# Performance work log

Hardware: AMD Instinct MI355X
Metric: run time of the kernel (lower is better)

Reference implementation:

```python
import jax, jax.numpy as jnp
import numpy as np

D_MODEL = 1024
NUM_HEADS = 16
D_HEAD = D_MODEL // NUM_HEADS
B, S = 4, 2048


def setup_inputs() -> dict:
    key = jax.random.key(0)
    ks = jax.random.split(key, 11)
    s = 1.0 / np.sqrt(D_MODEL)
    inp = {
        "query": jax.random.normal(ks[0], (B, S, D_MODEL), jnp.float32),
        "key": jax.random.normal(ks[1], (B, S, D_MODEL), jnp.float32),
        "value": jax.random.normal(ks[2], (B, S, D_MODEL), jnp.float32),
        "Wq": jax.random.uniform(ks[3], (D_MODEL, D_MODEL), jnp.float32, -s, s),
        "bq": jax.random.uniform(ks[4], (D_MODEL,), jnp.float32, -s, s),
        "Wk": jax.random.uniform(ks[5], (D_MODEL, D_MODEL), jnp.float32, -s, s),
        "bk": jax.random.uniform(ks[6], (D_MODEL,), jnp.float32, -s, s),
        "Wv": jax.random.uniform(ks[7], (D_MODEL, D_MODEL), jnp.float32, -s, s),
        "bv": jax.random.uniform(ks[8], (D_MODEL,), jnp.float32, -s, s),
        "Wo": jax.random.uniform(ks[9], (D_MODEL, D_MODEL), jnp.float32, -s, s),
        "bo": jax.random.uniform(ks[10], (D_MODEL,), jnp.float32, -s, s),
    }
    return inp


def reference(query, key, value, Wq, bq, Wk, bk, Wv, bv, Wo, bo):
    # Linear projections (torch Linear: x @ W.T + b)
    q = query @ Wq.T + bq  # [B,S,D]
    k = key @ Wk.T + bk
    v = value @ Wv.T + bv
    # split heads -> [B,H,S,Dh]
    def split(x):
        return x.reshape(B, S, NUM_HEADS, D_HEAD).transpose(0, 2, 1, 3)
    q, k, v = split(q), split(k), split(v)
    scale = 1.0 / np.sqrt(D_HEAD).astype(np.float32)
    scores = jnp.einsum('bhqd,bhkd->bhqk', q, k) * scale
    attn = jax.nn.softmax(scores, axis=-1)  # dropout is identity in eval
    ctx = jnp.einsum('bhqk,bhkd->bhqd', attn, v)
    ctx = ctx.transpose(0, 2, 1, 3).reshape(B, S, D_MODEL)
    return ctx @ Wo.T + bo
```

## Files before the change

kernel.cpp:

```cpp
#include <hip/hip_runtime.h>
#include <hip/hip_bf16.h>

typedef __bf16 bf16;
typedef bf16 bf16x8 __attribute__((ext_vector_type(8)));
typedef float f32x4 __attribute__((ext_vector_type(4)));
typedef float f32x16 __attribute__((ext_vector_type(16)));
typedef unsigned int u32x2 __attribute__((ext_vector_type(2)));
typedef unsigned int u32x4 __attribute__((ext_vector_type(4)));

#define B_  4
#define S_  2048
#define DM  1024
#define NH  16
#define DH  64

#define QSCALE 0.18033688011112042f


__device__ __forceinline__ void async_copy16(const void* g, void* lds) {
    __builtin_amdgcn_global_load_lds(
        (const __attribute__((address_space(1))) void*)g,
        (__attribute__((address_space(3))) void*)lds,
        16, 0, 0);
}

__device__ __forceinline__ bf16x8 read_frag(const char* lds, int row, int kbyte) {
    int off = row * 128 + (kbyte ^ ((row & 7) << 4));
    return *(const bf16x8*)(lds + off);
}

template<int ROWS, int NT>
__device__ __forceinline__ void stage_g2l(const bf16* g, int gs, char* lds) {
    int t = threadIdx.x;
#pragma unroll
    for (int i = 0; i < ROWS * 8 / NT; ++i) {
        int c = i * NT + t;
        int r = c >> 3;
        int s = (c & 7) ^ (r & 7);
        async_copy16(g + (long)r * gs + s * 8, lds + c * 16);
    }
}

__device__ __forceinline__ void stage_f32_g2l(const float* g, int gs, char* lds) {
    int t = threadIdx.x;
#pragma unroll
    for (int i = 0; i < 8; ++i) {
        int c = i * 256 + t;
        int r = c >> 4;
        int ch = c & 15;
        int sch = ch ^ (r & 15);
        async_copy16(g + (long)r * gs + sch * 4, lds + c * 16);
    }
}

__device__ __forceinline__ unsigned cvt_pk(float lo, float hi) {
    unsigned r;
    asm("v_cvt_pk_bf16_f32 %0, %1, %2" : "=v"(r) : "v"(lo), "v"(hi));
    return r;
}

__device__ __forceinline__ bf16x8 read_frag_f32(const char* lds, int row, int ks, int seg) {
    int ch0 = ks * 8 + seg * 2;
    int sw = row & 15;
    const char* base = lds + row * 256;
    f32x4 lo = *(const f32x4*)(base + ((ch0 ^ sw) * 16));
    f32x4 hi = *(const f32x4*)(base + (((ch0 + 1) ^ sw) * 16));
    u32x4 w;
    w.x = cvt_pk(lo[0], lo[1]);
    w.y = cvt_pk(lo[2], lo[3]);
    w.z = cvt_pk(hi[0], hi[1]);
    w.w = cvt_pk(hi[2], hi[3]);
    return __builtin_bit_cast(bf16x8, w);
}

__device__ __forceinline__ u32x2 pl32swap(unsigned a, unsigned b) {
    return __builtin_amdgcn_permlane32_swap(a, b, false, false);
}


__device__ __forceinline__ void cvt_body(const float* __restrict__ s, bf16* __restrict__ d, int n8) {
    for (int i = blockIdx.x * 256 + threadIdx.x; i < n8; i += gridDim.x * 256) {
        f32x4 v0 = *(const f32x4*)(s + (long)i * 8);
        f32x4 v1 = *(const f32x4*)(s + (long)i * 8 + 4);
        bf16x8 r;
#pragma unroll
        for (int j = 0; j < 4; ++j) { r[j] = (bf16)v0[j]; r[j + 4] = (bf16)v1[j]; }
        *(bf16x8*)(d + (long)i * 8) = r;
    }
}

__global__ __launch_bounds__(256) void cvt_w(
    const float* __restrict__ a, const float* __restrict__ b,
    const float* __restrict__ c, const float* __restrict__ d,
    bf16* __restrict__ oa, bf16* __restrict__ ob, bf16* __restrict__ oc, bf16* __restrict__ od)
{
    int z = blockIdx.y;
    cvt_body(z == 0 ? a : z == 1 ? b : z == 2 ? c : d,
             z == 0 ? oa : z == 1 ? ob : z == 2 ? oc : od, DM * DM / 8);
}

__global__ __launch_bounds__(256) void qkv_gemm(
    const float* __restrict__ xq, const float* __restrict__ xk, const float* __restrict__ xv,
    const bf16* __restrict__ wq, const bf16* __restrict__ wk, const bf16* __restrict__ wv,
    const float* __restrict__ bq, const float* __restrict__ bk, const float* __restrict__ bv,
    bf16* __restrict__ qo, bf16* __restrict__ ko, bf16* __restrict__ vo)
{
    __shared__ alignas(128) char As[128 * 256];
    __shared__ alignas(128) char Bs[128 * 128];

    int z = blockIdx.y;
    const float* X    = (z == 0) ? xq : (z == 1) ? xk : xv;
    const bf16* W     = (z == 0) ? wq : (z == 1) ? wk : wv;
    const float* bias = (z == 0) ? bq : (z == 1) ? bk : bv;
    bf16* out         = (z == 0) ? qo : (z == 1) ? ko : vo;
    float scale       = (z == 0) ? QSCALE : 1.0f;
    bool  vt          = (z == 2);

    int p = blockIdx.x;
    int xcd = p & 7, slot = p >> 3;
    int m0 = (xcd * 8 + (slot >> 3)) * 128;
    int n0 = (slot & 7) * 128;

    int lane = threadIdx.x & 63, wid = threadIdx.x >> 6;
    int wm = (wid >> 1) * 64, wn = (wid & 1) * 64;
    int seg = lane >> 4;

    f32x4 acc[4][4];
#pragma unroll
    for (int i = 0; i < 4; ++i)
#pragma unroll
        for (int j = 0; j < 4; ++j) acc[i][j] = f32x4{0.f, 0.f, 0.f, 0.f};

    for (int k0 = 0; k0 < DM; k0 += 64) {
        __syncthreads();
        stage_f32_g2l(X + (long)m0 * DM + k0, DM, As);
        stage_g2l<128, 256>(W + (long)n0 * DM + k0, DM, Bs);
        __syncthreads();
#pragma unroll
        for (int ks = 0; ks < 2; ++ks) {
            int kb = ks * 64 + seg * 16;
            bf16x8 af[4], bfr[4];
#pragma unroll
            for (int f = 0; f < 4; ++f)
                af[f] = read_frag_f32(As, wm + f * 16 + (lane & 15), ks, seg);
#pragma unroll
            for (int f = 0; f < 4; ++f)
                bfr[f] = read_frag(Bs, wn + f * 16 + (lane & 15), kb);
#pragma unroll
            for (int mf = 0; mf < 4; ++mf)
#pragma unroll
                for (int nf = 0; nf < 4; ++nf)
                    acc[mf][nf] = __builtin_amdgcn_mfma_f32_16x16x32_bf16(
                        af[mf], bfr[nf], acc[mf][nf], 0, 0, 0);
        }
    }

#pragma unroll
    for (int nf = 0; nf < 4; ++nf) {
        int j = n0 + wn + nf * 16 + (lane & 15);
        float bj = bias[j];
        int h = j >> 6, dh = j & 63;
#pragma unroll
        for (int mf = 0; mf < 4; ++mf) {
#pragma unroll
            for (int r = 0; r < 4; ++r) {
                int i = m0 + wm + mf * 16 + (lane >> 4) * 4 + r;
                float v = (acc[mf][nf][r] + bj) * scale;
                int b = i >> 11, s = i & 2047;
                long addr = vt ? ((long)((b * NH + h) * DH + dh)) * S_ + s
                               : ((long)((b * NH + h) * S_ + s)) * DH + dh;
                out[addr] = (bf16)v;
            }
        }
    }
}

__global__ __launch_bounds__(256) void out_gemm(
    const bf16* __restrict__ ctxb, const bf16* __restrict__ wo, const float* __restrict__ bo,
    float* __restrict__ out)
{
    __shared__ alignas(128) char As[128 * 128];
    __shared__ alignas(128) char Bs[128 * 128];

    int p = blockIdx.x;
    int xcd = p & 7, slot = p >> 3;
    int m0 = (xcd * 8 + (slot >> 3)) * 128;
    int n0 = (slot & 7) * 128;

    int lane = threadIdx.x & 63, wid = threadIdx.x >> 6;
    int wm = (wid >> 1) * 64, wn = (wid & 1) * 64;

    f32x4 acc[4][4];
#pragma unroll
    for (int i = 0; i < 4; ++i)
#pragma unroll
        for (int j = 0; j < 4; ++j) acc[i][j] = f32x4{0.f, 0.f, 0.f, 0.f};

    for (int k0 = 0; k0 < DM; k0 += 64) {
        __syncthreads();
        stage_g2l<128, 256>(ctxb + (long)m0 * DM + k0, DM, As);
        stage_g2l<128, 256>(wo + (long)n0 * DM + k0, DM, Bs);
        __syncthreads();
#pragma unroll
        for (int ks = 0; ks < 2; ++ks) {
            int kb = ks * 64 + (lane >> 4) * 16;
            bf16x8 af[4], bfr[4];
#pragma unroll
            for (int f = 0; f < 4; ++f) af[f]  = read_frag(As, wm + f * 16 + (lane & 15), kb);
#pragma unroll
            for (int f = 0; f < 4; ++f) bfr[f] = read_frag(Bs, wn + f * 16 + (lane & 15), kb);
#pragma unroll
            for (int mf = 0; mf < 4; ++mf)
#pragma unroll
                for (int nf = 0; nf < 4; ++nf)
                    acc[mf][nf] = __builtin_amdgcn_mfma_f32_16x16x32_bf16(
                        af[mf], bfr[nf], acc[mf][nf], 0, 0, 0);
        }
    }

#pragma unroll
    for (int nf = 0; nf < 4; ++nf) {
        int j = n0 + wn + nf * 16 + (lane & 15);
        float bj = bo[j];
#pragma unroll
        for (int mf = 0; mf < 4; ++mf)
#pragma unroll
            for (int r = 0; r < 4; ++r) {
                int i = m0 + wm + mf * 16 + (lane >> 4) * 4 + r;
                out[(long)i * DM + j] = acc[mf][nf][r] + bj;
            }
    }
}

__global__ __launch_bounds__(256) void attn_fwd(
    const bf16* __restrict__ qb, const bf16* __restrict__ kb, const bf16* __restrict__ vtb,
    bf16* __restrict__ ctx)
{
    __shared__ alignas(128) char Ks[2][64 * 128];
    __shared__ alignas(128) char Vs[2][64 * 128];

    int bid = blockIdx.x;
    int xcd = bid & 7, rest = bid >> 3;
    int qt = rest & 15, bh = xcd + 8 * (rest >> 4);

    int lane = threadIdx.x & 63, wid = threadIdx.x >> 6;
    int ln = lane & 31, h = lane >> 5;
    int q0w = qt * 128 + wid * 32;

    const bf16* qg = qb + (long)bh * S_ * DH;
    const bf16* kg = kb + (long)bh * S_ * DH;
    const bf16* vg = vtb + (long)bh * DH * S_;

    bf16x8 qf[4];
#pragma unroll
    for (int s = 0; s < 4; ++s)
        qf[s] = *(const bf16x8*)(qg + (long)(q0w + ln) * DH + s * 16 + h * 8);

    const bf16x8 onea = __builtin_bit_cast(bf16x8,
        u32x4{0x3F803F80u, 0x3F803F80u, 0x3F803F80u, 0x3F803F80u});

    f32x16 fz;
#pragma unroll
    for (int r = 0; r < 16; ++r) fz[r] = 0.f;

    f32x16 o[2];
#pragma unroll
    for (int t = 0; t < 2; ++t)
#pragma unroll
        for (int r = 0; r < 16; ++r) o[t][r] = 0.f;
    f32x16 lacc;
#pragma unroll
    for (int r = 0; r < 16; ++r) lacc[r] = 0.f;

    stage_g2l<64, 256>(kg, DH, Ks[0]);
    stage_g2l<64, 256>(vg, S_, Vs[0]);
    __syncthreads();

    int cur = 0;
    for (int kt2 = 0; kt2 < S_ / 64; ++kt2) {
        f32x16 acc[2];
        __builtin_amdgcn_s_setprio(1);
#pragma unroll
        for (int t = 0; t < 2; ++t) {
            bf16x8 ka = read_frag(Ks[cur], 32 * t + ln, 16 * h);
            acc[t] = __builtin_amdgcn_mfma_f32_32x32x16_bf16(ka, qf[0], fz, 0, 0, 0);
        }
#pragma unroll
        for (int s = 1; s < 4; ++s)
#pragma unroll
            for (int t = 0; t < 2; ++t) {
                bf16x8 ka = read_frag(Ks[cur], 32 * t + ln, 32 * s + 16 * h);
                acc[t] = __builtin_amdgcn_mfma_f32_32x32x16_bf16(ka, qf[s], acc[t], 0, 0, 0);
            }
        __builtin_amdgcn_s_setprio(0);

        if (kt2 + 1 < S_ / 64) {
            stage_g2l<64, 256>(kg + (long)(kt2 + 1) * 64 * DH, DH, Ks[cur ^ 1]);
            stage_g2l<64, 256>(vg + (kt2 + 1) * 64, S_, Vs[cur ^ 1]);
        }

#pragma unroll
        for (int t = 0; t < 2; ++t)
#pragma unroll
            for (int r = 0; r < 16; ++r)
                acc[t][r] = __builtin_amdgcn_exp2f(acc[t][r]);

        unsigned pf[4][4];
#pragma unroll
        for (int t = 0; t < 2; ++t)
#pragma unroll
            for (int hf = 0; hf < 2; ++hf) {
                int rb = 8 * hf;
                unsigned a0 = cvt_pk(acc[t][rb + 0], acc[t][rb + 1]);
                unsigned s0 = cvt_pk(acc[t][rb + 4], acc[t][rb + 5]);
                unsigned a1 = cvt_pk(acc[t][rb + 2], acc[t][rb + 3]);
                unsigned s1 = cvt_pk(acc[t][rb + 6], acc[t][rb + 7]);
                u32x2 r0 = pl32swap(a0, s0);
                u32x2 r1 = pl32swap(a1, s1);
                int kt = 2 * t + hf;
                pf[kt][0] = r0.x; pf[kt][2] = r0.y;
                pf[kt][1] = r1.x; pf[kt][3] = r1.y;
            }

        __builtin_amdgcn_s_setprio(1);
#pragma unroll
        for (int kt = 0; kt < 4; ++kt) {
            bf16x8 pb = __builtin_bit_cast(bf16x8,
                u32x4{pf[kt][0], pf[kt][1], pf[kt][2], pf[kt][3]});
            bf16x8 va0 = read_frag(Vs[cur], ln,      32 * kt + 16 * h);
            o[0] = __builtin_amdgcn_mfma_f32_32x32x16_bf16(va0, pb, o[0], 0, 0, 0);
            bf16x8 va1 = read_frag(Vs[cur], 32 + ln, 32 * kt + 16 * h);
            o[1] = __builtin_amdgcn_mfma_f32_32x32x16_bf16(va1, pb, o[1], 0, 0, 0);
            lacc = __builtin_amdgcn_mfma_f32_32x32x16_bf16(onea, pb, lacc, 0, 0, 0);
        }
        __builtin_amdgcn_s_setprio(0);

        __syncthreads();
        cur ^= 1;
    }

    int b = bh >> 4, head = bh & 15;
    float inv = 1.0f / lacc[0];
    int s = q0w + ln;
    bf16* base = ctx + ((long)(b * S_ + s)) * DM + head * DH;
#pragma unroll
    for (int dt = 0; dt < 2; ++dt)
#pragma unroll
        for (int c = 0; c < 4; ++c) {
            int d0 = 32 * dt + 8 * c + 4 * h;
            u32x2 st;
            st.x = cvt_pk(o[dt][4 * c + 0] * inv, o[dt][4 * c + 1] * inv);
            st.y = cvt_pk(o[dt][4 * c + 2] * inv, o[dt][4 * c + 3] * inv);
            *(u32x2*)(base + d0) = st;
        }
}

extern "C" void kernel_launch(void* const* d_in, const int* in_sizes, int n_in,
                              void* d_out, int out_size, void* d_ws, size_t ws_size,
                              hipStream_t stream) {
    const float* query = (const float*)d_in[0];
    const float* key   = (const float*)d_in[1];
    const float* value = (const float*)d_in[2];
    const float* Wq = (const float*)d_in[3];
    const float* bq = (const float*)d_in[4];
    const float* Wk = (const float*)d_in[5];
    const float* bk = (const float*)d_in[6];
    const float* Wv = (const float*)d_in[7];
    const float* bv = (const float*)d_in[8];
    const float* Wo = (const float*)d_in[9];
    const float* bo = (const float*)d_in[10];
    float* out = (float*)d_out;

    char* ws = (char*)d_ws;
    const long MB = 1ll << 20;
    bf16* qb   = (bf16*)(ws + 0 * MB);
    bf16* kb   = (bf16*)(ws + 16 * MB);
    bf16* vtb  = (bf16*)(ws + 32 * MB);
    bf16* ctxb = (bf16*)(ws + 48 * MB);
    bf16* wqb  = (bf16*)(ws + 64 * MB);
    bf16* wkb  = (bf16*)(ws + 66 * MB);
    bf16* wvb  = (bf16*)(ws + 68 * MB);
    bf16* wob  = (bf16*)(ws + 70 * MB);

    dim3 blk(256);
    cvt_w<<<dim3(512, 4), blk, 0, stream>>>(Wq, Wk, Wv, Wo, wqb, wkb, wvb, wob);
    qkv_gemm<<<dim3(512, 3), blk, 0, stream>>>(query, key, value, wqb, wkb, wvb,
                                               bq, bk, bv, qb, kb, vtb);
    attn_fwd<<<dim3(1024), blk, 0, stream>>>(qb, kb, vtb, ctxb);
    out_gemm<<<dim3(512), blk, 0, stream>>>(ctxb, wob, bo, out);
}
```

Baseline: 215.8 us.

## Software-pipeline attention loop: compute next QK^T while doing current PV

Restructures the attention main loop so the QK^T MFMAs for tile t+1 are issued alongside the PV MFMAs for tile t. The exp2 and bf16 packing of the next tile then happen after the barrier, and the prefetch is issued two tiles ahead into the freed buffer. The aim is to overlap the exp/convert VALU work and the load latency with matrix-core work. In exchange it needs more registers for the extra accumulator set, which could lower occupancy.

New measurement: 209.4 us, median of 2. -2.9%, faster.

```diff
diff --git a/kernel.cpp b/kernel.cpp
--- a/kernel.cpp
+++ b/kernel.cpp
@@ -275,54 +275,67 @@
     stage_g2l<64, 256>(kg, DH, Ks[0]);
     stage_g2l<64, 256>(vg, S_, Vs[0]);
     __syncthreads();
-
-    int cur = 0;
-    for (int kt2 = 0; kt2 < S_ / 64; ++kt2) {
-        f32x16 acc[2];
+    stage_g2l<64, 256>(kg + (long)64 * DH, DH, Ks[1]);
+    stage_g2l<64, 256>(vg + 64, S_, Vs[1]);
+
+    f32x16 acc2[2];
+    __builtin_amdgcn_s_setprio(1);
+#pragma unroll
+    for (int t = 0; t < 2; ++t) {
+        bf16x8 ka = read_frag(Ks[0], 32 * t + ln, 16 * h);
+        acc2[t] = __builtin_amdgcn_mfma_f32_32x32x16_bf16(ka, qf[0], fz, 0, 0, 0);
+    }
+#pragma unroll
+    for (int s = 1; s < 4; ++s)
+#pragma unroll
+        for (int t = 0; t < 2; ++t) {
+            bf16x8 ka = read_frag(Ks[0], 32 * t + ln, 32 * s + 16 * h);
+            acc2[t] = __builtin_amdgcn_mfma_f32_32x32x16_bf16(ka, qf[s], acc2[t], 0, 0, 0);
+        }
+    __builtin_amdgcn_s_setprio(0);
+
+    unsigned pf[4][4];
+#pragma unroll
+    for (int t = 0; t < 2; ++t)
+#pragma unroll
+        for (int r = 0; r < 16; ++r)
+            acc2[t][r] = __builtin_amdgcn_exp2f(acc2[t][r]);
+#pragma unroll
+    for (int t = 0; t < 2; ++t)
+#pragma unroll
+        for (int hf = 0; hf < 2; ++hf) {
+            int rb = 8 * hf;
+            unsigned a0 = cvt_pk(acc2[t][rb + 0], acc2[t][rb + 1]);
+            unsigned s0 = cvt_pk(acc2[t][rb + 4], acc2[t][rb + 5]);
+            unsigned a1 = cvt_pk(acc2[t][rb + 2], acc2[t][rb + 3]);
+            unsigned s1 = cvt_pk(acc2[t][rb + 6], acc2[t][rb + 7]);
+            u32x2 r0 = pl32swap(a0, s0);
+            u32x2 r1 = pl32swap(a1, s1);
+            int kt = 2 * t + hf;
+            pf[kt][0] = r0.x; pf[kt][2] = r0.y;
+            pf[kt][1] = r1.x; pf[kt][3] = r1.y;
+        }
+
+    const int NT = S_ / 64;
+    for (int t = 0; t < NT; ++t) {
+        int cur = t & 1, nxt = cur ^ 1;
+        __syncthreads();
+
         __builtin_amdgcn_s_setprio(1);
-#pragma unroll
-        for (int t = 0; t < 2; ++t) {
-            bf16x8 ka = read_frag(Ks[cur], 32 * t + ln, 16 * h);
-            acc[t] = __builtin_amdgcn_mfma_f32_32x32x16_bf16(ka, qf[0], fz, 0, 0, 0);
-        }
-#pragma unroll
-        for (int s = 1; s < 4; ++s)
-#pragma unroll
-            for (int t = 0; t < 2; ++t) {
-                bf16x8 ka = read_frag(Ks[cur], 32 * t + ln, 32 * s + 16 * h);
-                acc[t] = __builtin_amdgcn_mfma_f32_32x32x16_bf16(ka, qf[s], acc[t], 0, 0, 0);
+        if (t + 1 < NT) {
+#pragma unroll
+            for (int tt = 0; tt < 2; ++tt) {
+                bf16x8 ka = read_frag(Ks[nxt], 32 * tt + ln, 16 * h);
+                acc2[tt] = __builtin_amdgcn_mfma_f32_32x32x16_bf16(ka, qf[0], fz, 0, 0, 0);
             }
-        __builtin_amdgcn_s_setprio(0);
-
-        if (kt2 + 1 < S_ / 64) {
-            stage_g2l<64, 256>(kg + (long)(kt2 + 1) * 64 * DH, DH, Ks[cur ^ 1]);
-            stage_g2l<64, 256>(vg + (kt2 + 1) * 64, S_, Vs[cur ^ 1]);
-        }
-
-#pragma unroll
-        for (int t = 0; t < 2; ++t)
-#pragma unroll
-            for (int r = 0; r < 16; ++r)
-                acc[t][r] = __builtin_amdgcn_exp2f(acc[t][r]);
-
-        unsigned pf[4][4];
-#pragma unroll
-        for (int t = 0; t < 2; ++t)
-#pragma unroll
-            for (int hf = 0; hf < 2; ++hf) {
-                int rb = 8 * hf;
-                unsigned a0 = cvt_pk(acc[t][rb + 0], acc[t][rb + 1]);
-                unsigned s0 = cvt_pk(acc[t][rb + 4], acc[t][rb + 5]);
-                unsigned a1 = cvt_pk(acc[t][rb + 2], acc[t][rb + 3]);
-                unsigned s1 = cvt_pk(acc[t][rb + 6], acc[t][rb + 7]);
-                u32x2 r0 = pl32swap(a0, s0);
-                u32x2 r1 = pl32swap(a1, s1);
-                int kt = 2 * t + hf;
-                pf[kt][0] = r0.x; pf[kt][2] = r0.y;
-                pf[kt][1] = r1.x; pf[kt][3] = r1.y;
-            }
-
-        __builtin_amdgcn_s_setprio(1);
+#pragma unroll
+            for (int s = 1; s < 4; ++s)
+#pragma unroll
+                for (int tt = 0; tt < 2; ++tt) {
+                    bf16x8 ka = read_frag(Ks[nxt], 32 * tt + ln, 32 * s + 16 * h);
+                    acc2[tt] = __builtin_amdgcn_mfma_f32_32x32x16_bf16(ka, qf[s], acc2[tt], 0, 0, 0);
+                }
+        }
 #pragma unroll
         for (int kt = 0; kt < 4; ++kt) {
             bf16x8 pb = __builtin_bit_cast(bf16x8,
@@ -336,7 +349,34 @@
         __builtin_amdgcn_s_setprio(0);
 
         __syncthreads();
-        cur ^= 1;
+
+        if (t + 2 < NT) {
+            stage_g2l<64, 256>(kg + (long)(t + 2) * 64 * DH, DH, Ks[cur]);
+            stage_g2l<64, 256>(vg + (t + 2) * 64, S_, Vs[cur]);
+        }
+
+        if (t + 1 < NT) {
+#pragma unroll
+            for (int tt = 0; tt < 2; ++tt)
+#pragma unroll
+                for (int r = 0; r < 16; ++r)
+                    acc2[tt][r] = __builtin_amdgcn_exp2f(acc2[tt][r]);
+#pragma unroll
+            for (int tt = 0; tt < 2; ++tt)
+#pragma unroll
+                for (int hf = 0; hf < 2; ++hf) {
+                    int rb = 8 * hf;
+                    unsigned a0 = cvt_pk(acc2[tt][rb + 0], acc2[tt][rb + 1]);
+                    unsigned s0 = cvt_pk(acc2[tt][rb + 4], acc2[tt][rb + 5]);
+                    unsigned a1 = cvt_pk(acc2[tt][rb + 2], acc2[tt][rb + 3]);
+                    unsigned s1 = cvt_pk(acc2[tt][rb + 6], acc2[tt][rb + 7]);
+                    u32x2 r0 = pl32swap(a0, s0);
+                    u32x2 r1 = pl32swap(a1, s1);
+                    int kt = 2 * tt + hf;
+                    pf[kt][0] = r0.x; pf[kt][2] = r0.y;
+                    pf[kt][1] = r1.x; pf[kt][3] = r1.y;
+                }
+        }
     }
 
     int b = bh >> 4, head = bh & 15;
```

## Process two query tiles per attention block to reuse staged K/V tiles

Applied to the files above, without the earlier changes.

Each attention workgroup now handles 256 queries (two 32-row query fragments per wave) instead of 128, so every K/V tile staged into LDS feeds twice as many MFMAs. The grid is halved from 1024 to 512 blocks. The K/V prefetch is also restructured: the next tile is issued after the barrier, two tiles ahead, rather than mid-iteration. This cuts LDS fragment reads and global K/V traffic per query, at the cost of higher register pressure (doubled accumulators), lower occupancy, and fewer blocks to spread across CUs.

Result: slower. 235.2 us (+9.0%).

```diff
diff --git a/kernel.cpp b/kernel.cpp
--- a/kernel.cpp
+++ b/kernel.cpp
@@ -241,20 +241,23 @@
 
     int bid = blockIdx.x;
     int xcd = bid & 7, rest = bid >> 3;
-    int qt = rest & 15, bh = xcd + 8 * (rest >> 4);
+    int qt = rest & 7, bh = xcd + 8 * (rest >> 3);
 
     int lane = threadIdx.x & 63, wid = threadIdx.x >> 6;
     int ln = lane & 31, h = lane >> 5;
-    int q0w = qt * 128 + wid * 32;
+    int q0a = qt * 256 + wid * 32;
+    int q0b = q0a + 128;
 
     const bf16* qg = qb + (long)bh * S_ * DH;
     const bf16* kg = kb + (long)bh * S_ * DH;
     const bf16* vg = vtb + (long)bh * DH * S_;
 
-    bf16x8 qf[4];
-#pragma unroll
-    for (int s = 0; s < 4; ++s)
-        qf[s] = *(const bf16x8*)(qg + (long)(q0w + ln) * DH + s * 16 + h * 8);
+    bf16x8 qfa[4], qfb[4];
+#pragma unroll
+    for (int s = 0; s < 4; ++s) {
+        qfa[s] = *(const bf16x8*)(qg + (long)(q0a + ln) * DH + s * 16 + h * 8);
+        qfb[s] = *(const bf16x8*)(qg + (long)(q0b + ln) * DH + s * 16 + h * 8);
+    }
 
     const bf16x8 onea = __builtin_bit_cast(bf16x8,
         u32x4{0x3F803F80u, 0x3F803F80u, 0x3F803F80u, 0x3F803F80u});
@@ -263,95 +266,122 @@
 #pragma unroll
     for (int r = 0; r < 16; ++r) fz[r] = 0.f;
 
-    f32x16 o[2];
+    f32x16 oa[2], ob[2], la, lb;
+#pragma unroll
+    for (int r = 0; r < 16; ++r) { la[r] = 0.f; lb[r] = 0.f; }
 #pragma unroll
     for (int t = 0; t < 2; ++t)
 #pragma unroll
-        for (int r = 0; r < 16; ++r) o[t][r] = 0.f;
-    f32x16 lacc;
-#pragma unroll
-    for (int r = 0; r < 16; ++r) lacc[r] = 0.f;
+        for (int r = 0; r < 16; ++r) { oa[t][r] = 0.f; ob[t][r] = 0.f; }
 
     stage_g2l<64, 256>(kg, DH, Ks[0]);
     stage_g2l<64, 256>(vg, S_, Vs[0]);
     __syncthreads();
-
-    int cur = 0;
-    for (int kt2 = 0; kt2 < S_ / 64; ++kt2) {
-        f32x16 acc[2];
+    stage_g2l<64, 256>(kg + (long)64 * DH, DH, Ks[1]);
+    stage_g2l<64, 256>(vg + 64, S_, Vs[1]);
+
+    const int NT = S_ / 64;
+    for (int t = 0; t < NT; ++t) {
+        int cur = t & 1;
+        __syncthreads();
+
+        f32x16 aa[2], ab[2];
         __builtin_amdgcn_s_setprio(1);
 #pragma unroll
-        for (int t = 0; t < 2; ++t) {
-            bf16x8 ka = read_frag(Ks[cur], 32 * t + ln, 16 * h);
-            acc[t] = __builtin_amdgcn_mfma_f32_32x32x16_bf16(ka, qf[0], fz, 0, 0, 0);
+        for (int tt = 0; tt < 2; ++tt) {
+            bf16x8 ka = read_frag(Ks[cur], 32 * tt + ln, 16 * h);
+            aa[tt] = __builtin_amdgcn_mfma_f32_32x32x16_bf16(ka, qfa[0], fz, 0, 0, 0);
+            ab[tt] = __builtin_amdgcn_mfma_f32_32x32x16_bf16(ka, qfb[0], fz, 0, 0, 0);
         }
 #pragma unroll
         for (int s = 1; s < 4; ++s)
 #pragma unroll
-            for (int t = 0; t < 2; ++t) {
-                bf16x8 ka = read_frag(Ks[cur], 32 * t + ln, 32 * s + 16 * h);
-                acc[t] = __builtin_amdgcn_mfma_f32_32x32x16_bf16(ka, qf[s], acc[t], 0, 0, 0);
+            for (int tt = 0; tt < 2; ++tt) {
+                bf16x8 ka = read_frag(Ks[cur], 32 * tt + ln, 32 * s + 16 * h);
+                aa[tt] = __builtin_amdgcn_mfma_f32_32x32x16_bf16(ka, qfa[s], aa[tt], 0, 0, 0);
+                ab[tt] = __builtin_amdgcn_mfma_f32_32x32x16_bf16(ka, qfb[s], ab[tt], 0, 0, 0);
             }
         __builtin_amdgcn_s_setprio(0);
 
-        if (kt2 + 1 < S_ / 64) {
-            stage_g2l<64, 256>(kg + (long)(kt2 + 1) * 64 * DH, DH, Ks[cur ^ 1]);
-            stage_g2l<64, 256>(vg + (kt2 + 1) * 64, S_, Vs[cur ^ 1]);
-        }
-
-#pragma unroll
-        for (int t = 0; t < 2; ++t)
-#pragma unroll
-            for (int r = 0; r < 16; ++r)
-                acc[t][r] = __builtin_amdgcn_exp2f(acc[t][r]);
-
-        unsigned pf[4][4];
-#pragma unroll
-        for (int t = 0; t < 2; ++t)
+        unsigned pfa[4][4], pfb[4][4];
+#pragma unroll
+        for (int tt = 0; tt < 2; ++tt)
+#pragma unroll
+            for (int r = 0; r < 16; ++r) {
+                aa[tt][r] = __builtin_amdgcn_exp2f(aa[tt][r]);
+                ab[tt][r] = __builtin_amdgcn_exp2f(ab[tt][r]);
+            }
+#pragma unroll
+        for (int tt = 0; tt < 2; ++tt)
 #pragma unroll
             for (int hf = 0; hf < 2; ++hf) {
                 int rb = 8 * hf;
-                unsigned a0 = cvt_pk(acc[t][rb + 0], acc[t][rb + 1]);
-                unsigned s0 = cvt_pk(acc[t][rb + 4], acc[t][rb + 5]);
-                unsigned a1 = cvt_pk(acc[t][rb + 2], acc[t][rb + 3]);
-                unsigned s1 = cvt_pk(acc[t][rb + 6], acc[t][rb + 7]);
-                u32x2 r0 = pl32swap(a0, s0);
-                u32x2 r1 = pl32swap(a1, s1);
-                int kt = 2 * t + hf;
-                pf[kt][0] = r0.x; pf[kt][2] = r0.y;
-                pf[kt][1] = r1.x; pf[kt][3] = r1.y;
+                int kt = 2 * tt + hf;
+                {
+                    unsigned a0 = cvt_pk(aa[tt][rb + 0], aa[tt][rb + 1]);
+                    unsigned s0 = cvt_pk(aa[tt][rb + 4], aa[tt][rb + 5]);
+                    unsigned a1 = cvt_pk(aa[tt][rb + 2], aa[tt][rb + 3]);
+                    unsigned s1 = cvt_pk(aa[tt][rb + 6], aa[tt][rb + 7]);
+                    u32x2 r0 = pl32swap(a0, s0);
+                    u32x2 r1 = pl32swap(a1, s1);
+                    pfa[kt][0] = r0.x; pfa[kt][2] = r0.y;
+                    pfa[kt][1] = r1.x; pfa[kt][3] = r1.y;
+                }
+                {
+                    unsigned a0 = cvt_pk(ab[tt][rb + 0], ab[tt][rb + 1]);
+                    unsigned s0 = cvt_pk(ab[tt][rb + 4], ab[tt][rb + 5]);
+                    unsigned a1 = cvt_pk(ab[tt][rb + 2], ab[tt][rb + 3]);
+                    unsigned s1 = cvt_pk(ab[tt][rb + 6], ab[tt][rb + 7]);
+                    u32x2 r0 = pl32swap(a0, s0);
+                    u32x2 r1 = pl32swap(a1, s1);
+                    pfb[kt][0] = r0.x; pfb[kt][2] = r0.y;
+                    pfb[kt][1] = r1.x; pfb[kt][3] = r1.y;
+                }
             }
 
         __builtin_amdgcn_s_setprio(1);
 #pragma unroll
         for (int kt = 0; kt < 4; ++kt) {
-            bf16x8 pb = __builtin_bit_cast(bf16x8,
-                u32x4{pf[kt][0], pf[kt][1], pf[kt][2], pf[kt][3]});
+            bf16x8 pba = __builtin_bit_cast(bf16x8,
+                u32x4{pfa[kt][0], pfa[kt][1], pfa[kt][2], pfa[kt][3]});
+            bf16x8 pbb = __builtin_bit_cast(bf16x8,
+                u32x4{pfb[kt][0], pfb[kt][1], pfb[kt][2], pfb[kt][3]});
             bf16x8 va0 = read_frag(Vs[cur], ln,      32 * kt + 16 * h);
-            o[0] = __builtin_amdgcn_mfma_f32_32x32x16_bf16(va0, pb, o[0], 0, 0, 0);
+            oa[0] = __builtin_amdgcn_mfma_f32_32x32x16_bf16(va0, pba, oa[0], 0, 0, 0);
+            ob[0] = __builtin_amdgcn_mfma_f32_32x32x16_bf16(va0, pbb, ob[0], 0, 0, 0);
             bf16x8 va1 = read_frag(Vs[cur], 32 + ln, 32 * kt + 16 * h);
-            o[1] = __builtin_amdgcn_mfma_f32_32x32x16_bf16(va1, pb, o[1], 0, 0, 0);
-            lacc = __builtin_amdgcn_mfma_f32_32x32x16_bf16(onea, pb, lacc, 0, 0, 0);
+            oa[1] = __builtin_amdgcn_mfma_f32_32x32x16_bf16(va1, pba, oa[1], 0, 0, 0);
+            ob[1] = __builtin_amdgcn_mfma_f32_32x32x16_bf16(va1, pbb, ob[1], 0, 0, 0);
+            la = __builtin_amdgcn_mfma_f32_32x32x16_bf16(onea, pba, la, 0, 0, 0);
+            lb = __builtin_amdgcn_mfma_f32_32x32x16_bf16(onea, pbb, lb, 0, 0, 0);
         }
         __builtin_amdgcn_s_setprio(0);
 
         __syncthreads();
-        cur ^= 1;
+
+        if (t + 2 < NT) {
+            stage_g2l<64, 256>(kg + (long)(t + 2) * 64 * DH, DH, Ks[cur]);
+            stage_g2l<64, 256>(vg + (t + 2) * 64, S_, Vs[cur]);
+        }
     }
 
     int b = bh >> 4, head = bh & 15;
-    float inv = 1.0f / lacc[0];
-    int s = q0w + ln;
-    bf16* base = ctx + ((long)(b * S_ + s)) * DM + head * DH;
+    float inva = 1.0f / la[0];
+    float invb = 1.0f / lb[0];
+    bf16* base_a = ctx + ((long)(b * S_ + q0a + ln)) * DM + head * DH;
+    bf16* base_b = ctx + ((long)(b * S_ + q0b + ln)) * DM + head * DH;
 #pragma unroll
     for (int dt = 0; dt < 2; ++dt)
 #pragma unroll
         for (int c = 0; c < 4; ++c) {
             int d0 = 32 * dt + 8 * c + 4 * h;
             u32x2 st;
-            st.x = cvt_pk(o[dt][4 * c + 0] * inv, o[dt][4 * c + 1] * inv);
-            st.y = cvt_pk(o[dt][4 * c + 2] * inv, o[dt][4 * c + 3] * inv);
-            *(u32x2*)(base + d0) = st;
+            st.x = cvt_pk(oa[dt][4 * c + 0] * inva, oa[dt][4 * c + 1] * inva);
+            st.y = cvt_pk(oa[dt][4 * c + 2] * inva, oa[dt][4 * c + 3] * inva);
+            *(u32x2*)(base_a + d0) = st;
+            st.x = cvt_pk(ob[dt][4 * c + 0] * invb, ob[dt][4 * c + 1] * invb);
+            st.y = cvt_pk(ob[dt][4 * c + 2] * invb, ob[dt][4 * c + 3] * invb);
+            *(u32x2*)(base_b + d0) = st;
         }
 }
 
@@ -386,6 +416,6 @@
     cvt_w<<<dim3(512, 4), blk, 0, stream>>>(Wq, Wk, Wv, Wo, wqb, wkb, wvb, wob);
     qkv_gemm<<<dim3(512, 3), blk, 0, stream>>>(query, key, value, wqb, wkb, wvb,
                                                bq, bk, bv, qb, kb, vtb);
-    attn_fwd<<<dim3(1024), blk, 0, stream>>>(qb, kb, vtb, ctxb);
+    attn_fwd<<<dim3(512), blk, 0, stream>>>(qb, kb, vtb, ctxb);
     out_gemm<<<dim3(512), blk, 0, stream>>>(ctxb, wob, bo, out);
 }
```
